# Kernel optimization log

Hardware: AMD Instinct MI355X
Metric: run time of the kernel (lower is better)

The kernel has to match this reference:

```python
import jax, jax.numpy as jnp
import numpy as np

B = 1024
NIF = 2048   # n_image_features
V = 10000    # vocab_size
E = 512      # embedding_dim
H = 1024     # hidden_size
L = 32       # max_sentence_length
ND = 3       # num distractors


def _lstm_cell(x, h, c, Wih, Whh, bih, bhh):
    # torch LSTMCell: gates ordered i, f, g, o
    g = x @ Wih.T + bih + h @ Whh.T + bhh
    i, f, gc, o = jnp.split(g, 4, axis=-1)
    c = jax.nn.sigmoid(f) * c + jax.nn.sigmoid(i) * jnp.tanh(gc)
    h = jax.nn.sigmoid(o) * jnp.tanh(c)
    return h, c


def setup_inputs() -> dict:
    key = jax.random.key(0)
    ks = jax.random.split(key, 20)
    s = 0.02
    inp = {
        "target": jax.random.normal(ks[0], (B, NIF), jnp.float32),
        "distractors": jax.random.normal(ks[1], (ND, B, NIF), jnp.float32),
        "start_token_idx": 1,
        "max_sentence_length": L,
        # Sender params
        "W_aff": s * jax.random.normal(ks[2], (H, NIF), jnp.float32),
        "b_aff": jnp.zeros((H,), jnp.float32),
        "emb_s": s * jax.random.normal(ks[3], (V, E), jnp.float32),
        "Wih_s": s * jax.random.normal(ks[4], (4 * H, E), jnp.float32),
        "Whh_s": s * jax.random.normal(ks[5], (4 * H, H), jnp.float32),
        "bih_s": jnp.zeros((4 * H,), jnp.float32),
        "bhh_s": jnp.zeros((4 * H,), jnp.float32),
        "Wp": s * jax.random.normal(ks[6], (V, H), jnp.float32),
        "bp": jnp.zeros((V,), jnp.float32),
        # Receiver params
        "emb_r": s * jax.random.normal(ks[7], (V, E), jnp.float32),
        "Wih_r": s * jax.random.normal(ks[8], (4 * H, E), jnp.float32),
        "Whh_r": s * jax.random.normal(ks[9], (4 * H, H), jnp.float32),
        "bih_r": jnp.zeros((4 * H,), jnp.float32),
        "bhh_r": jnp.zeros((4 * H,), jnp.float32),
        "W_out": s * jax.random.normal(ks[10], (NIF, H), jnp.float32),
        "b_out": jnp.zeros((NIF,), jnp.float32),
    }
    return inp


def reference(target, distractors, start_token_idx, max_sentence_length,
              W_aff, b_aff, emb_s, Wih_s, Whh_s, bih_s, bhh_s, Wp, bp,
              emb_r, Wih_r, Whh_r, bih_r, bhh_r, W_out, b_out):
    Bt = target.shape[0]

    # ---- Sender: greedy decode (eval-mode argmax, matching greedy=True) ----
    h0 = target @ W_aff.T + b_aff
    c0 = jnp.zeros_like(h0)
    w0 = emb_s[jnp.full((Bt,), start_token_idx, dtype=jnp.int32)]

    def send_step(carry, _):
        h, c, w = carry
        h, c = _lstm_cell(w, h, c, Wih_s, Whh_s, bih_s, bhh_s)
        logits = h @ Wp.T + bp                         # [B, V]
        idx = jnp.argmax(logits, axis=-1)              # greedy token
        logp = jnp.take_along_axis(jax.nn.log_softmax(logits, axis=-1),
                                   idx[:, None], axis=-1)[:, 0]
        w = emb_s[idx]
        return (h, c, w), (idx, logp)

    _, (message, logps) = jax.lax.scan(send_step, (h0, c0, w0), None,
                                       length=max_sentence_length)
    message = message.T            # [B, L]
    log_prob = logps[-1]           # log_prob of last sampled word, [B]

    # ---- Receiver: encode message ----
    hr = jnp.zeros((Bt, H), jnp.float32)
    cr = jnp.zeros((Bt, H), jnp.float32)

    def recv_step(carry, w_idx):
        h, c = carry
        h, c = _lstm_cell(emb_r[w_idx], h, c, Wih_r, Whh_r, bih_r, bhh_r)
        return (h, c), None

    (hr, cr), _ = jax.lax.scan(recv_step, (hr, cr), message.T)
    r = hr @ W_out.T + b_out       # [B, NIF]

    # ---- Hinge loss over distractors ----
    r_T = r.T                                       # [NIF, B]
    t_r = target @ r_T                              # [B, B]
    d_r = jnp.einsum('nbf,fc->nbc', distractors, r_T)  # [ND, B, B]
    loss = jnp.sum(jnp.maximum(0.0, 1.0 - t_r[None] + d_r), axis=0)  # [B, B]
    loss = -loss * log_prob        # broadcast [B] over last dim, as in torch
    return jnp.mean(loss)
```

## Files before the change

### kernel.cpp

```cpp
#include <hip/hip_runtime.h>
#include <hip/hip_bf16.h>
#include <cstdint>
#include <cstddef>

#define Bc   1024
#define NIFc 2048
#define Vc   10000
#define Ec   512
#define Hc   1024
#define Lc   32
#define NDc  3
#define G4c  4096
#define NTv  79
#define TMLD 80
#define XLD  3584
#define XOFF 512

typedef __attribute__((ext_vector_type(4))) float f32x4;
typedef __attribute__((ext_vector_type(8))) short s16x8;
typedef __attribute__((ext_vector_type(4))) short s16x4;

#define GBM 128
#define GBN 128
#define GBK 64

struct __align__(16) GemmSmem {
    __hip_bfloat16 As[GBM * GBK];
    __hip_bfloat16 Ws[GBN * GBK];
    float smax[GBM];
};

__device__ __forceinline__ void gld_lds16(void* lds, const void* g) {
    __builtin_amdgcn_global_load_lds(
        (const __attribute__((address_space(1))) unsigned int*)g,
        (__attribute__((address_space(3))) unsigned int*)lds,
        16, 0, 0);
}

template<int OBF>
__device__ __forceinline__ void gemm_body(
    GemmSmem& sm,
    const __hip_bfloat16* __restrict__ A, int lda,
    const __hip_bfloat16* __restrict__ W, int ldw,
// ... 66 lines not shown
                    acc[i][j] = __builtin_amdgcn_mfma_f32_16x16x32_bf16(
                        af[i], wf[j], acc[i][j], 0, 0, 0);
        }
    }

    float rowmax[4][4];
    #pragma unroll
    for (int i = 0; i < 4; ++i)
        #pragma unroll
        for (int rr = 0; rr < 4; ++rr)
            rowmax[i][rr] = -__builtin_inff();

    #pragma unroll
    for (int i = 0; i < 4; ++i) {
        int mbase = m0 + hm + i * 16 + quad * 4;
        #pragma unroll
        for (int j = 0; j < 4; ++j) {
            int n = n0 + hn + j * 16 + lm;
            if (n < N) {
                float bv = bias ? bias[n] : 0.0f;
                #pragma unroll
                for (int rr = 0; rr < 4; ++rr) {
                    float v = acc[i][j][rr] + bv;
                    if (mbase + rr < M) {
                        if (OBF)
                            ((__hip_bfloat16*)Cv)[(size_t)(mbase + rr) * N + n] =
                                __float2bfloat16(v);
                        else
                            ((float*)Cv)[(size_t)(mbase + rr) * N + n] = v;
                    }
                    rowmax[i][rr] = fmaxf(rowmax[i][rr], v);
                }
            }
        }
    }

    if (tile_max) {
        #pragma unroll
        for (int i = 0; i < 4; ++i)
            #pragma unroll
            for (int rr = 0; rr < 4; ++rr) {
                float v = rowmax[i][rr];
                v = fmaxf(v, __shfl_xor(v, 1));
                v = fmaxf(v, __shfl_xor(v, 2));
                v = fmaxf(v, __shfl_xor(v, 4));
                v = fmaxf(v, __shfl_xor(v, 8));
                rowmax[i][rr] = v;
            }
        __syncthreads();
        if (hn == 0 && lm == 0) {
            #pragma unroll
            for (int i = 0; i < 4; ++i)
                #pragma unroll
                for (int rr = 0; rr < 4; ++rr)
                    smax[hm + i * 16 + quad * 4 + rr] = rowmax[i][rr];
        }
        __syncthreads();
        if (hn == 64 && lm == 0) {
            #pragma unroll
            for (int i = 0; i < 4; ++i)
                #pragma unroll
                for (int rr = 0; rr < 4; ++rr) {
                    int r = hm + i * 16 + quad * 4 + rr;
                    smax[r] = fmaxf(smax[r], rowmax[i][rr]);
                }
        }
        __syncthreads();
        if (tid < GBM)
            tile_max[(size_t)(m0 + tid) * tmld + bx] = smax[tid];
    }
}

__global__ __launch_bounds__(256) void gemm_bf16_tn(
    const __hip_bfloat16* __restrict__ A, int lda,
    const __hip_bfloat16* __restrict__ W, int ldw,
    const float* __restrict__ bias, float* __restrict__ C,
    int M, int N, int K, float* __restrict__ tile_max, int tmld)
{
    __shared__ GemmSmem sm;
    gemm_body<0>(sm, A, lda, W, ldw, bias, C, M, N, K, blockIdx.x, blockIdx.y,
                 tile_max, tmld);
}

__global__ __launch_bounds__(256) void gemm_bf16_obf(
    const __hip_bfloat16* __restrict__ A, int lda,
    const __hip_bfloat16* __restrict__ W, int ldw,
    __hip_bfloat16* __restrict__ C, int M, int N, int K)
{
    __shared__ GemmSmem sm;
    gemm_body<1>(sm, A, lda, W, ldw, nullptr, C, M, N, K, blockIdx.x,
                 blockIdx.y, nullptr, 0);
}

__global__ __launch_bounds__(256) void gemm_bf16_sk2(
    const __hip_bfloat16* __restrict__ A, int lda,
    const __hip_bfloat16* __restrict__ W, int ldw,
    float* __restrict__ Cpart, int M, int N, int Ksub)
{
    __shared__ GemmSmem sm;
    int z = blockIdx.z;
    gemm_body<0>(sm, A + (size_t)z * Ksub, lda, W + (size_t)z * Ksub, ldw,
                 nullptr, Cpart + (size_t)z * M * N, M, N, Ksub, blockIdx.x,
                 blockIdx.y, nullptr, 0);
}

__global__ __launch_bounds__(256) void gemm_fused_step(
    int nb_g, int nb_l,
    const __hip_bfloat16* __restrict__ Ag, const __hip_bfloat16* __restrict__ Wg,
    float* __restrict__ Cg,
    const __hip_bfloat16* __restrict__ Al, const __hip_bfloat16* __restrict__ Wl,
    const float* __restrict__ bl, float* __restrict__ Cl,
    float* __restrict__ tmax,
    const __hip_bfloat16* __restrict__ Ar, const __hip_bfloat16* __restrict__ Wr,
    float* __restrict__ Cr)
{
    __shared__ GemmSmem sm;
    int bid = blockIdx.x;
    if (bid < nb_g) {
        gemm_body<0>(sm, Ag, XLD, Wg, XLD, nullptr, Cg,
                     Bc, G4c, 3072, bid & 31, bid >> 5, nullptr, 0);
    } else if (bid < nb_g + nb_l) {
        int rem = bid - nb_g;
        int by = rem / NTv, bx = rem - by * NTv;
        gemm_body<0>(sm, Al, XLD, Wl, Hc, bl, Cl, Bc, Vc, Hc, bx, by,
                     tmax, TMLD);
    } else {
        int rem = bid - nb_g - nb_l;
        gemm_body<0>(sm, Ar, 1536, Wr, 1536, nullptr, Cr,
                     Bc, G4c, Hc, rem & 31, rem >> 5, nullptr, 0);
    }
}

__global__ __launch_bounds__(256) void split3_a_kernel(
    const float* __restrict__ in, int ldin,
    __hip_bfloat16* __restrict__ out, int ldo, int coff, int M, int K)
{
    int i = blockIdx.x * 256 + threadIdx.x;
    if (i >= M * K) return;
    int m = i / K, k = i - m * K;
    float v = in[(size_t)m * ldin + k];
    __hip_bfloat16 hi = __float2bfloat16(v);
    float lo = v - __bfloat162float(hi);
    __hip_bfloat16* row = out + (size_t)m * ldo + coff;
    row[k] = hi;
    row[K + k] = __float2bfloat16(lo);
    row[2 * K + k] = hi;
}

__global__ __launch_bounds__(256) void split3_w_kernel(
    const float* __restrict__ in, int ldin,
    __hip_bfloat16* __restrict__ out, int ldo, int coff, int M, int K)
{
    int i = blockIdx.x * 256 + threadIdx.x;
    if (i >= M * K) return;
    int m = i / K, k = i - m * K;
    float v = in[(size_t)m * ldin + k];
    __hip_bfloat16 hi = __float2bfloat16(v);
    float lo = v - __bfloat162float(hi);
    __hip_bfloat16* row = out + (size_t)m * ldo + coff;
    row[k] = hi;
    row[K + k] = hi;
    row[2 * K + k] = __float2bfloat16(lo);
}

__global__ __launch_bounds__(256) void cast2d_kernel(
    const float* __restrict__ in, int ldin,
    __hip_bfloat16* __restrict__ out, int ldo, int coff, int M, int K)
{
    int i = blockIdx.x * 256 + threadIdx.x;
    if (i >= M * K) return;
    int m = i / K, k = i - m * K;
    out[(size_t)m * ldo + coff + k] = __float2bfloat16(in[(size_t)m * ldin + k]);
}

__global__ __launch_bounds__(256) void gather_cast_kernel(
    const float* __restrict__ emb, int E, const int* __restrict__ idx,
    int stride, __hip_bfloat16* __restrict__ out, int ldo, int coff, int Brows)
{
    int i = blockIdx.x * 256 + threadIdx.x;
    if (i >= Brows * E) return;
    int b = i / E, k = i - b * E;
    out[(size_t)b * ldo + coff + k] =
        __float2bfloat16(emb[(size_t)idx[(size_t)b * stride] * E + k]);
}

__global__ __launch_bounds__(256) void add_vec_kernel(
    const float* __restrict__ a, const float* __restrict__ b,
    float* __restrict__ o, int n)
{
    int i = blockIdx.x * 256 + threadIdx.x;
    if (i < n) o[i] = a[i] + b[i];
}

__device__ __forceinline__ short bf16bits(float x) {
    __hip_bfloat16 t = __float2bfloat16(x);
    return *reinterpret_cast<short*>(&t);
}

__device__ __forceinline__ float b16f(short s) {
    return __bfloat162float(*reinterpret_cast<__hip_bfloat16*>(&s));
}

__global__ __launch_bounds__(256) void lstm_fused_s(
    const float* __restrict__ gp0, const float* __restrict__ gp1,
    const float* __restrict__ bias, float* __restrict__ h,
    float* __restrict__ c, __hip_bfloat16* __restrict__ h3x,
    const __hip_bfloat16* __restrict__ xg, const int* __restrict__ tok,
    int tstride)
{
    int i = blockIdx.x * 256 + threadIdx.x;
    if (i >= Bc * Hc / 4) return;
    int b = i >> 8;
    int j = (i & 255) * 4;
    size_t g0 = (size_t)b * G4c + j;
// ... 59 lines not shown
    s16x4 hi4, lo4;
    #pragma unroll
    for (int k = 0; k < 4; ++k) {
        hi4[k] = bf16bits(v[k]);
        lo4[k] = bf16bits(v[k] - __bfloat162float(__float2bfloat16(v[k])));
    }
    __hip_bfloat16* row = h3x + (size_t)b * XLD + XOFF;
    *(s16x4*)(row + j) = hi4;
    *(s16x4*)(row + Hc + j) = lo4;
    *(s16x4*)(row + 2 * Hc + j) = hi4;
}

__global__ __launch_bounds__(256) void lstm_fused_r(
    const float* __restrict__ gp0, const float* __restrict__ gp1,
    const float* __restrict__ bias, float* __restrict__ h,
    float* __restrict__ c, __hip_bfloat16* __restrict__ xh_r,
    const __hip_bfloat16* __restrict__ xg, const int* __restrict__ tok,
    int has_g, const float* __restrict__ emb, const int* __restrict__ msg_next)
{
    int i = blockIdx.x * 256 + threadIdx.x;
    if (i >= Bc * Hc / 4) return;
    int b = i >> 8;
    int j = (i & 255) * 4;
    f32x4 gi = *(const f32x4*)(bias + j);
    f32x4 gf = *(const f32x4*)(bias + Hc + j);
    f32x4 gg = *(const f32x4*)(bias + 2 * Hc + j);
    f32x4 go = *(const f32x4*)(bias + 3 * Hc + j);
    if (has_g) {
        size_t g0 = (size_t)b * G4c + j;
        gi += *(const f32x4*)(gp0 + g0) + *(const f32x4*)(gp1 + g0);
        gf += *(const f32x4*)(gp0 + g0 + Hc) + *(const f32x4*)(gp1 + g0 + Hc);
        gg += *(const f32x4*)(gp0 + g0 + 2 * Hc) + *(const f32x4*)(gp1 + g0 + 2 * Hc);
        go += *(const f32x4*)(gp0 + g0 + 3 * Hc) + *(const f32x4*)(gp1 + g0 + 3 * Hc);
    }
    if (xg) {
        const __hip_bfloat16* xr = xg + (size_t)tok[b] * G4c;
        s16x4 xi = *(const s16x4*)(xr + j);
        s16x4 xf = *(const s16x4*)(xr + Hc + j);
        s16x4 xc = *(const s16x4*)(xr + 2 * Hc + j);
        s16x4 xo = *(const s16x4*)(xr + 3 * Hc + j);
        #pragma unroll
        for (int k = 0; k < 4; ++k) {
            gi[k] += b16f(xi[k]);
            gf[k] += b16f(xf[k]);
            gg[k] += b16f(xc[k]);
            go[k] += b16f(xo[k]);
        }
    }
    size_t hix = (size_t)b * Hc + j;
    f32x4 cv = *(const f32x4*)(c + hix);
    f32x4 cn, hv;
    s16x4 hb4;
    #pragma unroll
    for (int k = 0; k < 4; ++k) {
        float si = 1.0f / (1.0f + expf(-gi[k]));
        float sf = 1.0f / (1.0f + expf(-gf[k]));
        float so = 1.0f / (1.0f + expf(-go[k]));
        float cc = sf * cv[k] + si * tanhf(gg[k]);
        cn[k] = cc;
        float hh = so * tanhf(cc);
        hv[k] = hh;
        hb4[k] = bf16bits(hh);
    }
    *(f32x4*)(c + hix) = cn;
    *(f32x4*)(h + hix) = hv;
    *(s16x4*)(xh_r + (size_t)b * 1536 + Ec + j) = hb4;
    if (!xg && msg_next && j < Ec) {
        int t2 = msg_next[b];
        f32x4 e = *(const f32x4*)(emb + (size_t)t2 * Ec + j);
        s16x4 eb;
        #pragma unroll
        for (int k = 0; k < 4; ++k) eb[k] = bf16bits(e[k]);
        *(s16x4*)(xh_r + (size_t)b * 1536 + j) = eb;
    }
}

__global__ __launch_bounds__(256) void argmax_rescore_v3(
    const float* __restrict__ logits, const float* __restrict__ tmax,
    const float* __restrict__ h, const float* __restrict__ Wp,
    const float* __restrict__ bp, const float* __restrict__ emb,
    int* __restrict__ msg_t, float* __restrict__ logp,
    __hip_bfloat16* __restrict__ xdst, int want_logp)
{
    const int b = blockIdx.x;
    const int tid = threadIdx.x;
    const int lane = tid & 63;
    const int wave = tid >> 6;
    const float* row = logits + (size_t)b * Vc;

    __shared__ float stm[128];
    __shared__ float redm[256];
    __shared__ float reds[256];
    __shared__ int   qt[32];
    __shared__ int   nq, cnt;
    __shared__ int   cand[64];
    __shared__ float score[64];
// ... 84 lines not shown
            f32x4 v = row4[j];
            s += expf(v.x - m) + expf(v.y - m) + expf(v.z - m) + expf(v.w - m);
        }
        redm[tid] = s;
        __syncthreads();
        #pragma unroll
        for (int st = 128; st > 0; st >>= 1) {
            if (tid < st) redm[tid] += redm[tid + st];
            __syncthreads();
        }
        if (tid == 0) logp[b] = sbestv - (m + logf(redm[0]));
    }

    if (xdst && tid < 128) {
        int k = tid * 4;
        f32x4 e = *(const f32x4*)(emb + (size_t)bestj * Ec + k);
        s16x4 h4;
        #pragma unroll
        for (int kk = 0; kk < 4; ++kk) h4[kk] = bf16bits(e[kk]);
        *(s16x4*)(xdst + (size_t)b * XLD + k) = h4;
    }
}

__global__ __launch_bounds__(256) void argmax_lstm_step(
    const float* __restrict__ logits, const float* __restrict__ tmax,
    const float* __restrict__ h, const float* __restrict__ Wp,
    const float* __restrict__ bp, int* __restrict__ msg_t,
    float* __restrict__ logp, int want_logp,
    int do_s, const float* __restrict__ gp0,
    const float* __restrict__ bias_s, float* __restrict__ h_s,
    float* __restrict__ c_s, __hip_bfloat16* __restrict__ h3x,
    const __hip_bfloat16* __restrict__ Xg_s,
    int has_gr, const float* __restrict__ gr0,
    const float* __restrict__ bias_r, float* __restrict__ hr,
    float* __restrict__ cr, __hip_bfloat16* __restrict__ xh_r,
    const __hip_bfloat16* __restrict__ Xg_r)
{
    const int b = blockIdx.x;
    const int tid = threadIdx.x;
    const int lane = tid & 63;
    const int wave = tid >> 6;
    const float* row = logits + (size_t)b * Vc;

    __shared__ float stm[128];
    __shared__ float redm[256];
    __shared__ float reds[256];
    __shared__ int   qt[32];
    __shared__ int   nq, cnt;
    __shared__ int   cand[64];
    __shared__ float score[64];
    __shared__ float sbestv;
    __shared__ int   sbestj;

    float tv = (tid < NTv) ? tmax[(size_t)b * TMLD + tid] : -__builtin_inff();
    if (tid < 128) stm[tid] = tv;
    redm[tid] = tv;
    reds[tid] = (tid < NTv) ? tv : 0.0f;
    if (tid == 0) { nq = 0; cnt = 0; }
    __syncthreads();
    #pragma unroll
    for (int s = 128; s > 0; s >>= 1) {
        if (tid < s) {
            redm[tid] = fmaxf(redm[tid], redm[tid + s]);
            reds[tid] += reds[tid + s];
        }
        __syncthreads();
    }
    const float m = redm[0];
    const float spread = m - reds[0] * (1.0f / NTv);
    const float delta = 0.08f * spread + 1e-6f * (1.0f + fabsf(m));

    if (tid < NTv && stm[tid] >= m - delta) {
        int k = atomicAdd(&nq, 1);
        if (k < 32) qt[k] = tid;
    }
    __syncthreads();
    int nqt = nq < 32 ? nq : 32;

    for (int qi = 0; qi < nqt; qi += 2) {
        int ti = qi + (tid >> 7);
        if (ti < nqt) {
            int j = qt[ti] * 128 + (tid & 127);
            if (j < Vc) {
                float v = row[j];
                if (v >= m - delta) {
                    int k = atomicAdd(&cnt, 1);
                    if (k < 64) cand[k] = j;
                }
            }
        }
    }
    __syncthreads();
    int nc = cnt < 64 ? cnt : 64;

    const float* hrow = h + (size_t)b * Hc;
    for (int cix = wave; cix < nc; cix += 4) {
        int j = cand[cix];
        const float* wrow = Wp + (size_t)j * Hc;
        float part = 0.0f;
        #pragma unroll
        for (int kk = 0; kk < 4; ++kk) {
            int k = kk * 256 + lane * 4;
            f32x4 hv = *(const f32x4*)(hrow + k);
            f32x4 wv = *(const f32x4*)(wrow + k);
            part = fmaf(hv.x, wv.x, part);
            part = fmaf(hv.y, wv.y, part);
            part = fmaf(hv.z, wv.z, part);
            part = fmaf(hv.w, wv.w, part);
        }
        #pragma unroll
        for (int off = 1; off < 64; off <<= 1)
            part += __shfl_xor(part, off);
        if (lane == 0) score[cix] = part + bp[j];
    }
    __syncthreads();
    if (tid == 0) {
        float bv = -__builtin_inff();
        int bj = 0x7fffffff;
        for (int cix = 0; cix < nc; ++cix) {
            float v = score[cix];
            int j = cand[cix];
            if (v > bv || (v == bv && j < bj)) { bv = v; bj = j; }
        }
        sbestv = bv;
        sbestj = bj;
        msg_t[b] = bj;
    }
    __syncthreads();
    const int tok = sbestj;

    if (want_logp) {
        float s = 0.0f;
        const f32x4* row4 = (const f32x4*)row;
        for (int j = tid; j < Vc / 4; j += 256) {
            f32x4 v = row4[j];
            s += expf(v.x - m) + expf(v.y - m) + expf(v.z - m) + expf(v.w - m);
        }
        redm[tid] = s;
        __syncthreads();
        #pragma unroll
        for (int st = 128; st > 0; st >>= 1) {
            if (tid < st) redm[tid] += redm[tid + st];
            __syncthreads();
        }
        if (tid == 0) logp[b] = sbestv - (m + logf(redm[0]));
        __syncthreads();
    }

    const int j = tid * 4;

    if (do_s) {
        size_t g0 = (size_t)b * G4c + j;
        f32x4 gi = *(const f32x4*)(gp0 + g0) + *(const f32x4*)(bias_s + j);
        f32x4 gf = *(const f32x4*)(gp0 + g0 + Hc) + *(const f32x4*)(bias_s + Hc + j);
        f32x4 gg = *(const f32x4*)(gp0 + g0 + 2 * Hc) + *(const f32x4*)(bias_s + 2 * Hc + j);
        f32x4 go = *(const f32x4*)(gp0 + g0 + 3 * Hc) + *(const f32x4*)(bias_s + 3 * Hc + j);
        const __hip_bfloat16* xr = Xg_s + (size_t)tok * G4c;
        s16x4 xi = *(const s16x4*)(xr + j);
        s16x4 xf = *(const s16x4*)(xr + Hc + j);
        s16x4 xc = *(const s16x4*)(xr + 2 * Hc + j);
        s16x4 xo = *(const s16x4*)(xr + 3 * Hc + j);
        size_t hix = (size_t)b * Hc + j;
        f32x4 cv = *(const f32x4*)(c_s + hix);
        f32x4 cn, hv;
        s16x4 hi4, lo4;
        #pragma unroll
        for (int k = 0; k < 4; ++k) {
            float gik = gi[k] + b16f(xi[k]);
            float gfk = gf[k] + b16f(xf[k]);
            float ggk = gg[k] + b16f(xc[k]);
            float gok = go[k] + b16f(xo[k]);
            float si = 1.0f / (1.0f + expf(-gik));
            float sf = 1.0f / (1.0f + expf(-gfk));
            float so = 1.0f / (1.0f + expf(-gok));
            float cc = sf * cv[k] + si * tanhf(ggk);
            cn[k] = cc;
            float hh = so * tanhf(cc);
            hv[k] = hh;
            hi4[k] = bf16bits(hh);
            lo4[k] = bf16bits(hh - __bfloat162float(__float2bfloat16(hh)));
        }
        *(f32x4*)(c_s + hix) = cn;
        *(f32x4*)(h_s + hix) = hv;
        __hip_bfloat16* orow = h3x + (size_t)b * XLD + XOFF;
        *(s16x4*)(orow + j) = hi4;
        *(s16x4*)(orow + Hc + j) = lo4;
        *(s16x4*)(orow + 2 * Hc + j) = hi4;
    }

    {
        f32x4 gi = *(const f32x4*)(bias_r + j);
        f32x4 gf = *(const f32x4*)(bias_r + Hc + j);
        f32x4 gg = *(const f32x4*)(bias_r + 2 * Hc + j);
        f32x4 go = *(const f32x4*)(bias_r + 3 * Hc + j);
        if (has_gr) {
            size_t g0 = (size_t)b * G4c + j;
            gi += *(const f32x4*)(gr0 + g0);
            gf += *(const f32x4*)(gr0 + g0 + Hc);
            gg += *(const f32x4*)(gr0 + g0 + 2 * Hc);
            go += *(const f32x4*)(gr0 + g0 + 3 * Hc);
        }
        const __hip_bfloat16* xr = Xg_r + (size_t)tok * G4c;
        s16x4 xi = *(const s16x4*)(xr + j);
        s16x4 xf = *(const s16x4*)(xr + Hc + j);
        s16x4 xc = *(const s16x4*)(xr + 2 * Hc + j);
        s16x4 xo = *(const s16x4*)(xr + 3 * Hc + j);
        size_t hix = (size_t)b * Hc + j;
        f32x4 cv = *(const f32x4*)(cr + hix);
        f32x4 cn, hv;
        s16x4 hb4;
        #pragma unroll
        for (int k = 0; k < 4; ++k) {
            float gik = gi[k] + b16f(xi[k]);
            float gfk = gf[k] + b16f(xf[k]);
            float ggk = gg[k] + b16f(xc[k]);
            float gok = go[k] + b16f(xo[k]);
            float si = 1.0f / (1.0f + expf(-gik));
            float sf = 1.0f / (1.0f + expf(-gfk));
            float so = 1.0f / (1.0f + expf(-gok));
            float cc = sf * cv[k] + si * tanhf(ggk);
            cn[k] = cc;
            float hh = so * tanhf(cc);
            hv[k] = hh;
            hb4[k] = bf16bits(hh);
        }
        *(f32x4*)(cr + hix) = cn;
        *(f32x4*)(hr + hix) = hv;
        *(s16x4*)(xh_r + (size_t)b * 1536 + Ec + j) = hb4;
    }
}

__global__ __launch_bounds__(256) void hinge_kernel(
    const float* __restrict__ S, const float* __restrict__ logp,
    float* __restrict__ partials, int Bn)
{
    int tid = threadIdx.x;
    int n = Bn * Bn;
    float acc = 0.0f;
    for (int idx = blockIdx.x * 256 + tid; idx < n; idx += gridDim.x * 256) {
        int j = idx & (Bn - 1);
        float s0 = S[idx];
        float l = fmaxf(0.0f, 1.0f - s0 + S[n + idx])
                + fmaxf(0.0f, 1.0f - s0 + S[2 * n + idx])
                + fmaxf(0.0f, 1.0f - s0 + S[3 * n + idx]);
        acc += l * logp[j];
    }
    __shared__ float sv[256];
    sv[tid] = acc;
    __syncthreads();
    for (int s = 128; s > 0; s >>= 1) {
        if (tid < s) sv[tid] += sv[tid + s];
// ... 37 lines not shown
    const float* bhh_s = (const float*)d_in[10];
    const float* Wp    = (const float*)d_in[11];
    const float* bp    = (const float*)d_in[12];
    const float* emb_r = (const float*)d_in[13];
    const float* Wih_r = (const float*)d_in[14];
    const float* Whh_r = (const float*)d_in[15];
    const float* bih_r = (const float*)d_in[16];
    const float* bhh_r = (const float*)d_in[17];
    const float* W_out = (const float*)d_in[18];
    const float* b_out = (const float*)d_in[19];

    dim3 blk(256);

    char* b0 = (char*)d_ws;
    size_t off = 0;
    auto take = [&](size_t bytes) -> char* {
        char* p = b0 + off;
        off += (bytes + 511) & ~(size_t)511;
        return p;
    };
    const size_t MB = 1024 * 1024;
    __hip_bfloat16* W3x     = (__hip_bfloat16*)take((size_t)G4c * XLD * 2);
    __hip_bfloat16* Wp_b    = (__hip_bfloat16*)take((size_t)Vc * Hc * 2);
    __hip_bfloat16* WihWhh_r= (__hip_bfloat16*)take((size_t)G4c * 1536 * 2);
    __hip_bfloat16* W_out_b = (__hip_bfloat16*)take((size_t)NIFc * Hc * 2);
    __hip_bfloat16* h3x     = (__hip_bfloat16*)take((size_t)Bc * XLD * 2);
    __hip_bfloat16* xh_r    = (__hip_bfloat16*)take((size_t)Bc * 1536 * 2);
    float* gates_p = (float*)take((size_t)2 * Bc * G4c * 4);
    float* h_s    = (float*)take((size_t)Bc * Hc * 4);
    float* c_s    = (float*)take((size_t)Bc * Hc * 4);
    float* hr     = (float*)take((size_t)Bc * Hc * 4);
    float* cr     = (float*)take((size_t)Bc * Hc * 4);
    float* logp   = (float*)take(Bc * 4);
    int*   msg    = (int*)take((size_t)Lc * Bc * 4);
    float* parts  = (float*)take(1024 * 4);
    float* bias_s = (float*)take(G4c * 4);
    float* bias_r = (float*)take(G4c * 4);
    float* tilemax= (float*)take((size_t)Bc * TMLD * 4);
    char*  U      = take(48 * MB);

    __hip_bfloat16* Xg_s = (__hip_bfloat16*)take((size_t)Vc * G4c * 2);
    const int use_tab_s = (off <= ws_size);
    __hip_bfloat16* Xg_r = (__hip_bfloat16*)take((size_t)Vc * G4c * 2);
    const int use_tab_r = (off <= ws_size);
    const int use_merged = use_tab_s && use_tab_r;

    __hip_bfloat16* target3 = (__hip_bfloat16*)U;
    __hip_bfloat16* W_aff3  = (__hip_bfloat16*)(U + 13 * MB);
    __hip_bfloat16* emb_b   = (__hip_bfloat16*)(U + 26 * MB);
    float*          logits  = (float*)U;
    __hip_bfloat16* A4b     = (__hip_bfloat16*)U;
    float*          r_f     = (float*)(U + 17 * MB);
    __hip_bfloat16* r_b     = (__hip_bfloat16*)(U + 26 * MB);
    float*          S       = (float*)(U + 31 * MB);

    cast2d_kernel<<<(G4c * Ec + 255) / 256, blk, 0, stream>>>(
        Wih_s, Ec, W3x, XLD, 0, G4c, Ec);
    split3_w_kernel<<<(G4c * Hc + 255) / 256, blk, 0, stream>>>(
        Whh_s, Hc, W3x, XLD, XOFF, G4c, Hc);
    cast2d_kernel<<<(Vc * Hc + 255) / 256, blk, 0, stream>>>(
        Wp, Hc, Wp_b, Hc, 0, Vc, Hc);
    split3_a_kernel<<<(Bc * NIFc + 255) / 256, blk, 0, stream>>>(
        target, NIFc, target3, 6144, 0, Bc, NIFc);
    split3_w_kernel<<<(Hc * NIFc + 255) / 256, blk, 0, stream>>>(
        W_aff, NIFc, W_aff3, 6144, 0, Hc, NIFc);
    cast2d_kernel<<<(G4c * Ec + 255) / 256, blk, 0, stream>>>(
        Wih_r, Ec, WihWhh_r, 1536, 0, G4c, Ec);
    cast2d_kernel<<<(G4c * Hc + 255) / 256, blk, 0, stream>>>(
        Whh_r, Hc, WihWhh_r, 1536, Ec, G4c, Hc);
    cast2d_kernel<<<(NIFc * Hc + 255) / 256, blk, 0, stream>>>(
        W_out, Hc, W_out_b, Hc, 0, NIFc, Hc);
    add_vec_kernel<<<(G4c + 255) / 256, blk, 0, stream>>>(bih_s, bhh_s,
                                                          bias_s, G4c);
    add_vec_kernel<<<(G4c + 255) / 256, blk, 0, stream>>>(bih_r, bhh_r,
                                                          bias_r, G4c);

    if (use_tab_s) {
        cast2d_kernel<<<(Vc * Ec + 255) / 256, blk, 0, stream>>>(
            emb_s, Ec, emb_b, Ec, 0, Vc, Ec);
        gemm_bf16_obf<<<dim3(G4c / GBN, (Vc + GBM - 1) / GBM), blk, 0, stream>>>(
            emb_b, Ec, W3x, XLD, Xg_s, Vc, G4c, Ec);
    }
    if (use_tab_r) {
        cast2d_kernel<<<(Vc * Ec + 255) / 256, blk, 0, stream>>>(
            emb_r, Ec, emb_b, Ec, 0, Vc, Ec);
        gemm_bf16_obf<<<dim3(G4c / GBN, (Vc + GBM - 1) / GBM), blk, 0, stream>>>(
            emb_b, Ec, WihWhh_r, 1536, Xg_r, Vc, G4c, Ec);
    }

    gemm_bf16_sk2<<<dim3(Hc / GBN, Bc / GBM, 2), blk, 0, stream>>>(
        target3, 6144, W_aff3, 6144, gates_p, Bc, Hc, 3072);
    combine_h0_kernel<<<(Bc * Hc / 4 + 255) / 256, blk, 0, stream>>>(
        gates_p, gates_p + (size_t)Bc * Hc, b_aff, h_s, h3x);
    hipMemsetAsync(c_s, 0, (size_t)Bc * Hc * 4, stream);

    if (use_merged) {
        hipMemsetAsync(cr, 0, (size_t)Bc * Hc * 4, stream);

        gemm_bf16_sk2<<<dim3(G4c / GBN, Bc / GBM, 2), blk, 0, stream>>>(
            h3x + XOFF, XLD, W3x + XOFF, XLD, gates_p, Bc, G4c, 1536);
        lstm_fused_s<<<(Bc * Hc / 4 + 255) / 256, blk, 0, stream>>>(
            gates_p, gates_p + (size_t)Bc * G4c, bias_s, h_s, c_s, h3x,
            Xg_s, start_t, 0);

        float* gates_s = gates_p;
        float* gates_r = gates_p + (size_t)Bc * G4c;

        for (int t = 0; t < Lc; ++t) {
            const int nb_g = (t < Lc - 1) ? 256 : 0;
            const int nb_r = (t >= 1) ? 256 : 0;
            gemm_fused_step<<<nb_g + 632 + nb_r, blk, 0, stream>>>(
                nb_g, 632,
                h3x + XOFF, W3x + XOFF, gates_s,
                h3x + XOFF, Wp_b, bp, logits, tilemax,
                xh_r + Ec, WihWhh_r + Ec, gates_r);
            argmax_lstm_step<<<Bc, blk, 0, stream>>>(
                logits, tilemax, h_s, Wp, bp, msg + t * Bc, logp,
                (t == Lc - 1) ? 1 : 0,
                (t < Lc - 1) ? 1 : 0, gates_s, bias_s, h_s, c_s, h3x, Xg_s,
                (t >= 1) ? 1 : 0, gates_r, bias_r, hr, cr, xh_r, Xg_r);
        }
    } else {
        if (!use_tab_s)
            gather_cast_kernel<<<(Bc * Ec + 255) / 256, blk, 0, stream>>>(
                emb_s, Ec, start_t, 0, h3x, XLD, 0, Bc);

        for (int t = 0; t < Lc; ++t) {
            if (use_tab_s) {
                gemm_bf16_sk2<<<dim3(G4c / GBN, Bc / GBM, 2), blk, 0, stream>>>(
                    h3x + XOFF, XLD, W3x + XOFF, XLD, gates_p, Bc, G4c, 1536);
                lstm_fused_s<<<(Bc * Hc / 4 + 255) / 256, blk, 0, stream>>>(
                    gates_p, gates_p + (size_t)Bc * G4c, bias_s, h_s, c_s, h3x,
                    Xg_s, (t == 0) ? start_t : (msg + (t - 1) * Bc),
                    (t == 0) ? 0 : 1);
            } else {
                gemm_bf16_sk2<<<dim3(G4c / GBN, Bc / GBM, 2), blk, 0, stream>>>(
                    h3x, XLD, W3x, XLD, gates_p, Bc, G4c, 1792);
                lstm_fused_s<<<(Bc * Hc / 4 + 255) / 256, blk, 0, stream>>>(
                    gates_p, gates_p + (size_t)Bc * G4c, bias_s, h_s, c_s, h3x,
                    nullptr, nullptr, 0);
            }
            gemm_bf16_tn<<<dim3((Vc + GBN - 1) / GBN, Bc / GBM), blk, 0, stream>>>(
                h3x + XOFF, XLD, Wp_b, Hc, bp, logits, Bc, Vc, Hc, tilemax, TMLD);
            argmax_rescore_v3<<<Bc, blk, 0, stream>>>(
                logits, tilemax, h_s, Wp, bp, emb_s, msg + t * Bc, logp,
                (!use_tab_s && t < Lc - 1) ? h3x : nullptr,
                (t == Lc - 1) ? 1 : 0);
        }

        hipMemsetAsync(hr, 0, (size_t)Bc * Hc * 4, stream);
        hipMemsetAsync(cr, 0, (size_t)Bc * Hc * 4, stream);
        hipMemsetAsync(xh_r, 0, (size_t)Bc * 1536 * 2, stream);
        if (!use_tab_r)
            gather_cast_kernel<<<(Bc * Ec + 255) / 256, blk, 0, stream>>>(
                emb_r, Ec, msg, 1, xh_r, 1536, 0, Bc);
        for (int t = 0; t < Lc; ++t) {
            if (use_tab_r) {
                if (t > 0)
                    gemm_bf16_sk2<<<dim3(G4c / GBN, Bc / GBM, 2), blk, 0, stream>>>(
                        xh_r + Ec, 1536, WihWhh_r + Ec, 1536, gates_p, Bc, G4c, 512);
                lstm_fused_r<<<(Bc * Hc / 4 + 255) / 256, blk, 0, stream>>>(
                    gates_p, gates_p + (size_t)Bc * G4c, bias_r, hr, cr, xh_r,
                    Xg_r, msg + t * Bc, (t > 0) ? 1 : 0, nullptr, nullptr);
            } else {
                gemm_bf16_sk2<<<dim3(G4c / GBN, Bc / GBM, 2), blk, 0, stream>>>(
                    xh_r, 1536, WihWhh_r, 1536, gates_p, Bc, G4c, 768);
                lstm_fused_r<<<(Bc * Hc / 4 + 255) / 256, blk, 0, stream>>>(
                    gates_p, gates_p + (size_t)Bc * G4c, bias_r, hr, cr, xh_r,
                    nullptr, nullptr, 1, emb_r,
                    (t < Lc - 1) ? (msg + (t + 1) * Bc) : nullptr);
            }
        }
    }

    gemm_bf16_tn<<<dim3(NIFc / GBN, Bc / GBM), blk, 0, stream>>>(
        xh_r + Ec, 1536, W_out_b, Hc, b_out, r_f, Bc, NIFc, Hc, nullptr, 0);

    cast2d_kernel<<<(Bc * NIFc + 255) / 256, blk, 0, stream>>>(
        target, NIFc, A4b, NIFc, 0, Bc, NIFc);
    cast2d_kernel<<<(NDc * Bc * NIFc + 255) / 256, blk, 0, stream>>>(
        distr, NIFc, A4b + (size_t)Bc * NIFc, NIFc, 0, NDc * Bc, NIFc);
    cast2d_kernel<<<(Bc * NIFc + 255) / 256, blk, 0, stream>>>(
        r_f, NIFc, r_b, NIFc, 0, Bc, NIFc);
    gemm_bf16_tn<<<dim3(Bc / GBN, 4 * Bc / GBM), blk, 0, stream>>>(
        A4b, NIFc, r_b, NIFc, nullptr, S, 4 * Bc, Bc, NIFc, nullptr, 0);

    hinge_kernel<<<1024, blk, 0, stream>>>(S, logp, parts, Bc);
    final_reduce_kernel<<<1, blk, 0, stream>>>(
        parts, 1024, (float*)d_out, -1.0f / ((float)Bc * (float)Bc));
}
```

Before: 4.510 ms.

## Fuse receiver LSTM cell into gate GEMM epilogue and store sender logits as bf16

The receiver's gate weights are permuted so each 64-column GEMM tile holds all four gates for 16 hidden units. The LSTM cell update can then run in the GEMM epilogue, with ping-pong h buffers and a final standalone recv kernel. This removes the fp32 receiver gate round-trip and the receiver cell work in the argmax kernel. Sender logits for non-final steps are written as bf16, halving logit traffic, and the tile max is computed on rounded values. The trade-offs are bf16 rounding in the argmax candidate screen and a heavier epilogue with gathered Xg reads.

```diff
diff --git a/kernel.cpp b/kernel.cpp
--- a/kernel.cpp
+++ b/kernel.cpp
@@ -15,10 +15,15 @@
 #define TMLD 80
 #define XLD  3584
 #define XOFF 512
+#define RLD  1536
 
 typedef __attribute__((ext_vector_type(4))) float f32x4;
 typedef __attribute__((ext_vector_type(8))) short s16x8;
 typedef __attribute__((ext_vector_type(4))) short s16x4;
+
+__device__ __host__ __forceinline__ int rperm_orig(int p) {
+    return ((p >> 4) & 3) * Hc + (p >> 6) * 16 + (p & 15);
+}
 
 #define GBM 128
 #define GBN 128
@@ -131,14 +136,17 @@
                 #pragma unroll
                 for (int rr = 0; rr < 4; ++rr) {
                     float v = acc[i][j][rr] + bv;
-                    if (mbase + rr < M) {
-                        if (OBF)
-                            ((__hip_bfloat16*)Cv)[(size_t)(mbase + rr) * N + n] =
-                                __float2bfloat16(v);
-                        else
+                    float vs = v;
+                    if (OBF) {
+                        __hip_bfloat16 vb = __float2bfloat16(v);
+                        vs = __bfloat162float(vb);
+                        if (mbase + rr < M)
+                            ((__hip_bfloat16*)Cv)[(size_t)(mbase + rr) * N + n] = vb;
+                    } else {
+                        if (mbase + rr < M)
                             ((float*)Cv)[(size_t)(mbase + rr) * N + n] = v;
                     }
-                    rowmax[i][rr] = fmaxf(rowmax[i][rr], v);
+                    rowmax[i][rr] = fmaxf(rowmax[i][rr], vs);
                 }
             }
         }
@@ -180,6 +188,120 @@
     }
 }
 
+__device__ __forceinline__ void recv_gemm_cell_body(
+    GemmSmem& sm,
+    const __hip_bfloat16* __restrict__ A,
+    const __hip_bfloat16* __restrict__ W,
+    const float* __restrict__ biasp,
+    const __hip_bfloat16* __restrict__ Xg,
+    const int* __restrict__ tok,
+    float* __restrict__ cr,
+    __hip_bfloat16* __restrict__ xh_out,
+    int bx, int by)
+{
+    __hip_bfloat16* As = sm.As;
+    __hip_bfloat16* Ws = sm.Ws;
+
+    const int tid  = threadIdx.x;
+    const int lane = tid & 63;
+    const int wave = tid >> 6;
+    const int m0 = by * GBM;
+    const int n0 = bx * GBN;
+
+    const __hip_bfloat16* ag[4];
+    const __hip_bfloat16* wg[4];
+    #pragma unroll
+    for (int r = 0; r < 4; ++r) {
+        int p = r * 256 + tid;
+        int m = p >> 3;
+        int q = (p & 7) ^ (m & 7);
+        ag[r] = A + (size_t)(m0 + m) * RLD + q * 8;
+        wg[r] = W + (size_t)(n0 + m) * RLD + q * 8;
+    }
+
+    f32x4 acc[4][4];
+    #pragma unroll
+    for (int i = 0; i < 4; ++i)
+        #pragma unroll
+        for (int j = 0; j < 4; ++j)
+            acc[i][j] = (f32x4)(0.0f);
+
+    const int hm = (wave & 1) << 6;
+    const int hn = (wave >> 1) << 6;
+    const int lm = lane & 15;
+    const int quad = lane >> 4;
+
+    for (int kt = 0; kt < Hc / GBK; ++kt) {
+        __syncthreads();
+        #pragma unroll
+        for (int r = 0; r < 4; ++r) {
+            int ldsbase = (r * 256 + wave * 64) * 8;
+            gld_lds16(As + ldsbase, ag[r]);
+            gld_lds16(Ws + ldsbase, wg[r]);
+            ag[r] += GBK;
+            wg[r] += GBK;
+        }
+        __syncthreads();
+        #pragma unroll
+        for (int c = 0; c < 2; ++c) {
+            s16x8 af[4], wf[4];
+            int q = c * 4 + quad;
+            #pragma unroll
+            for (int i = 0; i < 4; ++i) {
+                int m = hm + i * 16 + lm;
+                af[i] = *(const s16x8*)(As + ((m << 3) + (q ^ (m & 7))) * 8);
+                int n = hn + i * 16 + lm;
+                wf[i] = *(const s16x8*)(Ws + ((n << 3) + (q ^ (n & 7))) * 8);
+            }
+            #pragma unroll
+            for (int i = 0; i < 4; ++i)
+                #pragma unroll
+                for (int j = 0; j < 4; ++j)
+                    acc[i][j] = __builtin_amdgcn_mfma_f32_16x16x32_bf16(
+                        af[i], wf[j], acc[i][j], 0, 0, 0);
+        }
+    }
+
+    const int u = ((n0 + hn) >> 6) * 16 + lm;
+    int pc[4];
+    float bv[4];
+    #pragma unroll
+    for (int g = 0; g < 4; ++g) {
+        pc[g] = n0 + hn + g * 16 + lm;
+        bv[g] = biasp[pc[g]];
+    }
+    #pragma unroll
+    for (int i = 0; i < 4; ++i) {
+        #pragma unroll
+        for (int rr = 0; rr < 4; ++rr) {
+            int b = m0 + hm + i * 16 + quad * 4 + rr;
+            const __hip_bfloat16* xr = Xg + (size_t)tok[b] * G4c;
+            float gi = acc[i][0][rr] + bv[0] + __bfloat162float(xr[pc[0]]);
+            float gf = acc[i][1][rr] + bv[1] + __bfloat162float(xr[pc[1]]);
+            float gg = acc[i][2][rr] + bv[2] + __bfloat162float(xr[pc[2]]);
+            float go = acc[i][3][rr] + bv[3] + __bfloat162float(xr[pc[3]]);
+            float si = 1.0f / (1.0f + expf(-gi));
+            float sf = 1.0f / (1.0f + expf(-gf));
+            float so = 1.0f / (1.0f + expf(-go));
+            size_t cix = (size_t)b * Hc + u;
+            float cc = sf * cr[cix] + si * tanhf(gg);
+            cr[cix] = cc;
+            xh_out[(size_t)b * RLD + Ec + u] = __float2bfloat16(so * tanhf(cc));
+        }
+    }
+}
+
+__global__ __launch_bounds__(256) void gemm_recv_final(
+    const __hip_bfloat16* __restrict__ A, const __hip_bfloat16* __restrict__ W,
+    const float* __restrict__ biasp, const __hip_bfloat16* __restrict__ Xg,
+    const int* __restrict__ tok, float* __restrict__ cr,
+    __hip_bfloat16* __restrict__ xh_out)
+{
+    __shared__ GemmSmem sm;
+    recv_gemm_cell_body(sm, A, W, biasp, Xg, tok, cr, xh_out,
+                        blockIdx.x & 31, blockIdx.x >> 5);
+}
+
 __global__ __launch_bounds__(256) void gemm_bf16_tn(
     const __hip_bfloat16* __restrict__ A, int lda,
     const __hip_bfloat16* __restrict__ W, int ldw,
@@ -213,30 +335,33 @@
                  blockIdx.y, nullptr, 0);
 }
 
+template<int LOGBF>
 __global__ __launch_bounds__(256) void gemm_fused_step(
-    int nb_g, int nb_l,
+    int nb_g,
     const __hip_bfloat16* __restrict__ Ag, const __hip_bfloat16* __restrict__ Wg,
     float* __restrict__ Cg,
     const __hip_bfloat16* __restrict__ Al, const __hip_bfloat16* __restrict__ Wl,
-    const float* __restrict__ bl, float* __restrict__ Cl,
+    const float* __restrict__ bl, void* __restrict__ Cl,
     float* __restrict__ tmax,
     const __hip_bfloat16* __restrict__ Ar, const __hip_bfloat16* __restrict__ Wr,
-    float* __restrict__ Cr)
+    const float* __restrict__ biasrp, const __hip_bfloat16* __restrict__ Xgr,
+    const int* __restrict__ tokr, float* __restrict__ cr,
+    __hip_bfloat16* __restrict__ xh_out)
 {
     __shared__ GemmSmem sm;
     int bid = blockIdx.x;
     if (bid < nb_g) {
         gemm_body<0>(sm, Ag, XLD, Wg, XLD, nullptr, Cg,
                      Bc, G4c, 3072, bid & 31, bid >> 5, nullptr, 0);
-    } else if (bid < nb_g + nb_l) {
+    } else if (bid < nb_g + 632) {
         int rem = bid - nb_g;
         int by = rem / NTv, bx = rem - by * NTv;
-        gemm_body<0>(sm, Al, XLD, Wl, Hc, bl, Cl, Bc, Vc, Hc, bx, by,
-                     tmax, TMLD);
+        gemm_body<LOGBF>(sm, Al, XLD, Wl, Hc, bl, Cl, Bc, Vc, Hc, bx, by,
+                         tmax, TMLD);
     } else {
-        int rem = bid - nb_g - nb_l;
-        gemm_body<0>(sm, Ar, 1536, Wr, 1536, nullptr, Cr,
-                     Bc, G4c, Hc, rem & 31, rem >> 5, nullptr, 0);
+        int rem = bid - nb_g - 632;
+        recv_gemm_cell_body(sm, Ar, Wr, biasrp, Xgr, tokr, cr, xh_out,
+                            rem & 31, rem >> 5);
     }
 }
 
@@ -282,6 +407,17 @@
     out[(size_t)m * ldo + coff + k] = __float2bfloat16(in[(size_t)m * ldin + k]);
 }
 
+__global__ __launch_bounds__(256) void cast2d_perm_kernel(
+    const float* __restrict__ in, int ldin,
+    __hip_bfloat16* __restrict__ out, int ldo, int coff, int M, int K)
+{
+    int i = blockIdx.x * 256 + threadIdx.x;
+    if (i >= M * K) return;
+    int p = i / K, k = i - p * K;
+    out[(size_t)p * ldo + coff + k] =
+        __float2bfloat16(in[(size_t)rperm_orig(p) * ldin + k]);
+}
+
 __global__ __launch_bounds__(256) void gather_cast_kernel(
     const float* __restrict__ emb, int E, const int* __restrict__ idx,
     int stride, __hip_bfloat16* __restrict__ out, int ldo, int coff, int Brows)
@@ -299,6 +435,14 @@
 {
     int i = blockIdx.x * 256 + threadIdx.x;
     if (i < n) o[i] = a[i] + b[i];
+}
+
+__global__ __launch_bounds__(256) void add_vec_perm_kernel(
+    const float* __restrict__ a, const float* __restrict__ b,
+    float* __restrict__ o, int n)
+{
+    int i = blockIdx.x * 256 + threadIdx.x;
+    if (i < n) { int s = rperm_orig(i); o[i] = a[s] + b[s]; }
 }
 
 __device__ __forceinline__ short bf16bits(float x) {
@@ -404,23 +548,24 @@
     if (i >= Bc * Hc / 4) return;
     int b = i >> 8;
     int j = (i & 255) * 4;
-    f32x4 gi = *(const f32x4*)(bias + j);
-    f32x4 gf = *(const f32x4*)(bias + Hc + j);
-    f32x4 gg = *(const f32x4*)(bias + 2 * Hc + j);
-    f32x4 go = *(const f32x4*)(bias + 3 * Hc + j);
+    int pb = (j >> 4) * 64 + (j & 15);
+    f32x4 gi = *(const f32x4*)(bias + pb);
+    f32x4 gf = *(const f32x4*)(bias + pb + 16);
+    f32x4 gg = *(const f32x4*)(bias + pb + 32);
+    f32x4 go = *(const f32x4*)(bias + pb + 48);
     if (has_g) {
-        size_t g0 = (size_t)b * G4c + j;
+        size_t g0 = (size_t)b * G4c + pb;
         gi += *(const f32x4*)(gp0 + g0) + *(const f32x4*)(gp1 + g0);
-        gf += *(const f32x4*)(gp0 + g0 + Hc) + *(const f32x4*)(gp1 + g0 + Hc);
-        gg += *(const f32x4*)(gp0 + g0 + 2 * Hc) + *(const f32x4*)(gp1 + g0 + 2 * Hc);
-        go += *(const f32x4*)(gp0 + g0 + 3 * Hc) + *(const f32x4*)(gp1 + g0 + 3 * Hc);
+        gf += *(const f32x4*)(gp0 + g0 + 16) + *(const f32x4*)(gp1 + g0 + 16);
+        gg += *(const f32x4*)(gp0 + g0 + 32) + *(const f32x4*)(gp1 + g0 + 32);
+        go += *(const f32x4*)(gp0 + g0 + 48) + *(const f32x4*)(gp1 + g0 + 48);
     }
     if (xg) {
         const __hip_bfloat16* xr = xg + (size_t)tok[b] * G4c;
-        s16x4 xi = *(const s16x4*)(xr + j);
-        s16x4 xf = *(const s16x4*)(xr + Hc + j);
-        s16x4 xc = *(const s16x4*)(xr + 2 * Hc + j);
-        s16x4 xo = *(const s16x4*)(xr + 3 * Hc + j);
+        s16x4 xi = *(const s16x4*)(xr + pb);
+        s16x4 xf = *(const s16x4*)(xr + pb + 16);
+        s16x4 xc = *(const s16x4*)(xr + pb + 32);
+        s16x4 xo = *(const s16x4*)(xr + pb + 48);
         #pragma unroll
         for (int k = 0; k < 4; ++k) {
             gi[k] += b16f(xi[k]);
@@ -446,14 +591,14 @@
     }
     *(f32x4*)(c + hix) = cn;
     *(f32x4*)(h + hix) = hv;
-    *(s16x4*)(xh_r + (size_t)b * 1536 + Ec + j) = hb4;
+    *(s16x4*)(xh_r + (size_t)b * RLD + Ec + j) = hb4;
     if (!xg && msg_next && j < Ec) {
         int t2 = msg_next[b];
         f32x4 e = *(const f32x4*)(emb + (size_t)t2 * Ec + j);
         s16x4 eb;
         #pragma unroll
         for (int k = 0; k < 4; ++k) eb[k] = bf16bits(e[k]);
-        *(s16x4*)(xh_r + (size_t)b * 1536 + j) = eb;
+        *(s16x4*)(xh_r + (size_t)b * RLD + j) = eb;
     }
 }
 
@@ -584,25 +729,23 @@
     }
 }
 
+template<int LGBF>
 __global__ __launch_bounds__(256) void argmax_lstm_step(
-    const float* __restrict__ logits, const float* __restrict__ tmax,
+    const void* __restrict__ logits_v, const float* __restrict__ tmax,
     const float* __restrict__ h, const float* __restrict__ Wp,
     const float* __restrict__ bp, int* __restrict__ msg_t,
     float* __restrict__ logp, int want_logp,
     int do_s, const float* __restrict__ gp0,
     const float* __restrict__ bias_s, float* __restrict__ h_s,
     float* __restrict__ c_s, __hip_bfloat16* __restrict__ h3x,
-    const __hip_bfloat16* __restrict__ Xg_s,
-    int has_gr, const float* __restrict__ gr0,
-    const float* __restrict__ bias_r, float* __restrict__ hr,
-    float* __restrict__ cr, __hip_bfloat16* __restrict__ xh_r,
-    const __hip_bfloat16* __restrict__ Xg_r)
+    const __hip_bfloat16* __restrict__ Xg_s)
 {
     const int b = blockIdx.x;
     const int tid = threadIdx.x;
     const int lane = tid & 63;
     const int wave = tid >> 6;
-    const float* row = logits + (size_t)b * Vc;
+    const __hip_bfloat16* rowb = (const __hip_bfloat16*)logits_v + (size_t)b * Vc;
+    const float* rowf = (const float*)logits_v + (size_t)b * Vc;
 
     __shared__ float stm[128];
     __shared__ float redm[256];
@@ -644,7 +787,7 @@
         if (ti < nqt) {
             int j = qt[ti] * 128 + (tid & 127);
             if (j < Vc) {
-                float v = row[j];
+                float v = LGBF ? __bfloat162float(rowb[j]) : rowf[j];
                 if (v >= m - delta) {
                     int k = atomicAdd(&cnt, 1);
                     if (k < 64) cand[k] = j;
@@ -691,9 +834,9 @@
     __syncthreads();
     const int tok = sbestj;
 
-    if (want_logp) {
+    if (!LGBF && want_logp) {
         float s = 0.0f;
-        const f32x4* row4 = (const f32x4*)row;
+        const f32x4* row4 = (const f32x4*)rowf;
         for (int j = tid; j < Vc / 4; j += 256) {
             f32x4 v = row4[j];
             s += expf(v.x - m) + expf(v.y - m) + expf(v.z - m) + expf(v.w - m);
@@ -709,9 +852,8 @@
         __syncthreads();
     }
 
-    const int j = tid * 4;
-
     if (do_s) {
+        const int j = tid * 4;
         size_t g0 = (size_t)b * G4c + j;
         f32x4 gi = *(const f32x4*)(gp0 + g0) + *(const f32x4*)(bias_s + j);
         f32x4 gf = *(const f32x4*)(gp0 + g0 + Hc) + *(const f32x4*)(bias_s + Hc + j);
@@ -748,47 +890,6 @@
         *(s16x4*)(orow + j) = hi4;
         *(s16x4*)(orow + Hc + j) = lo4;
         *(s16x4*)(orow + 2 * Hc + j) = hi4;
-    }
-
-    {
-        f32x4 gi = *(const f32x4*)(bias_r + j);
-        f32x4 gf = *(const f32x4*)(bias_r + Hc + j);
-        f32x4 gg = *(const f32x4*)(bias_r + 2 * Hc + j);
-        f32x4 go = *(const f32x4*)(bias_r + 3 * Hc + j);
-        if (has_gr) {
-            size_t g0 = (size_t)b * G4c + j;
-            gi += *(const f32x4*)(gr0 + g0);
-            gf += *(const f32x4*)(gr0 + g0 + Hc);
-            gg += *(const f32x4*)(gr0 + g0 + 2 * Hc);
-            go += *(const f32x4*)(gr0 + g0 + 3 * Hc);
-        }
-        const __hip_bfloat16* xr = Xg_r + (size_t)tok * G4c;
-        s16x4 xi = *(const s16x4*)(xr + j);
-        s16x4 xf = *(const s16x4*)(xr + Hc + j);
-        s16x4 xc = *(const s16x4*)(xr + 2 * Hc + j);
-        s16x4 xo = *(const s16x4*)(xr + 3 * Hc + j);
-        size_t hix = (size_t)b * Hc + j;
-        f32x4 cv = *(const f32x4*)(cr + hix);
-        f32x4 cn, hv;
-        s16x4 hb4;
-        #pragma unroll
-        for (int k = 0; k < 4; ++k) {
-            float gik = gi[k] + b16f(xi[k]);
-            float gfk = gf[k] + b16f(xf[k]);
-            float ggk = gg[k] + b16f(xc[k]);
-            float gok = go[k] + b16f(xo[k]);
-            float si = 1.0f / (1.0f + expf(-gik));
-            float sf = 1.0f / (1.0f + expf(-gfk));
-            float so = 1.0f / (1.0f + expf(-gok));
-            float cc = sf * cv[k] + si * tanhf(ggk);
-            cn[k] = cc;
-            float hh = so * tanhf(cc);
-            hv[k] = hh;
-            hb4[k] = bf16bits(hh);
-        }
-        *(f32x4*)(cr + hix) = cn;
-        *(f32x4*)(hr + hix) = hv;
-        *(s16x4*)(xh_r + (size_t)b * 1536 + Ec + j) = hb4;
     }
 }
 
@@ -872,10 +973,11 @@
     const size_t MB = 1024 * 1024;
     __hip_bfloat16* W3x     = (__hip_bfloat16*)take((size_t)G4c * XLD * 2);
     __hip_bfloat16* Wp_b    = (__hip_bfloat16*)take((size_t)Vc * Hc * 2);
-    __hip_bfloat16* WihWhh_r= (__hip_bfloat16*)take((size_t)G4c * 1536 * 2);
+    __hip_bfloat16* WihWhh_r= (__hip_bfloat16*)take((size_t)G4c * RLD * 2);
     __hip_bfloat16* W_out_b = (__hip_bfloat16*)take((size_t)NIFc * Hc * 2);
     __hip_bfloat16* h3x     = (__hip_bfloat16*)take((size_t)Bc * XLD * 2);
-    __hip_bfloat16* xh_r    = (__hip_bfloat16*)take((size_t)Bc * 1536 * 2);
+    __hip_bfloat16* xh_rA   = (__hip_bfloat16*)take((size_t)Bc * RLD * 2);
+    __hip_bfloat16* xh_rB   = (__hip_bfloat16*)take((size_t)Bc * RLD * 2);
     float* gates_p = (float*)take((size_t)2 * Bc * G4c * 4);
     float* h_s    = (float*)take((size_t)Bc * Hc * 4);
     float* c_s    = (float*)take((size_t)Bc * Hc * 4);
@@ -914,16 +1016,16 @@
         target, NIFc, target3, 6144, 0, Bc, NIFc);
     split3_w_kernel<<<(Hc * NIFc + 255) / 256, blk, 0, stream>>>(
         W_aff, NIFc, W_aff3, 6144, 0, Hc, NIFc);
-    cast2d_kernel<<<(G4c * Ec + 255) / 256, blk, 0, stream>>>(
-        Wih_r, Ec, WihWhh_r, 1536, 0, G4c, Ec);
-    cast2d_kernel<<<(G4c * Hc + 255) / 256, blk, 0, stream>>>(
-        Whh_r, Hc, WihWhh_r, 1536, Ec, G4c, Hc);
+    cast2d_perm_kernel<<<(G4c * Ec + 255) / 256, blk, 0, stream>>>(
+        Wih_r, Ec, WihWhh_r, RLD, 0, G4c, Ec);
+    cast2d_perm_kernel<<<(G4c * Hc + 255) / 256, blk, 0, stream>>>(
+        Whh_r, Hc, WihWhh_r, RLD, Ec, G4c, Hc);
     cast2d_kernel<<<(NIFc * Hc + 255) / 256, blk, 0, stream>>>(
         W_out, Hc, W_out_b, Hc, 0, NIFc, Hc);
     add_vec_kernel<<<(G4c + 255) / 256, blk, 0, stream>>>(bih_s, bhh_s,
                                                           bias_s, G4c);
-    add_vec_kernel<<<(G4c + 255) / 256, blk, 0, stream>>>(bih_r, bhh_r,
-                                                          bias_r, G4c);
+    add_vec_perm_kernel<<<(G4c + 255) / 256, blk, 0, stream>>>(bih_r, bhh_r,
+                                                               bias_r, G4c);
 
     if (use_tab_s) {
         cast2d_kernel<<<(Vc * Ec + 255) / 256, blk, 0, stream>>>(
@@ -935,7 +1037,7 @@
         cast2d_kernel<<<(Vc * Ec + 255) / 256, blk, 0, stream>>>(
             emb_r, Ec, emb_b, Ec, 0, Vc, Ec);
         gemm_bf16_obf<<<dim3(G4c / GBN, (Vc + GBM - 1) / GBM), blk, 0, stream>>>(
-            emb_b, Ec, WihWhh_r, 1536, Xg_r, Vc, G4c, Ec);
+            emb_b, Ec, WihWhh_r, RLD, Xg_r, Vc, G4c, Ec);
     }
 
     gemm_bf16_sk2<<<dim3(Hc / GBN, Bc / GBM, 2), blk, 0, stream>>>(
@@ -946,6 +1048,7 @@
 
     if (use_merged) {
         hipMemsetAsync(cr, 0, (size_t)Bc * Hc * 4, stream);
+        hipMemsetAsync(xh_rA, 0, (size_t)Bc * RLD * 2, stream);
 
         gemm_bf16_sk2<<<dim3(G4c / GBN, Bc / GBM, 2), blk, 0, stream>>>(
             h3x + XOFF, XLD, W3x + XOFF, XLD, gates_p, Bc, G4c, 1536);
@@ -953,23 +1056,38 @@
             gates_p, gates_p + (size_t)Bc * G4c, bias_s, h_s, c_s, h3x,
             Xg_s, start_t, 0);
 
-        float* gates_s = gates_p;
-        float* gates_r = gates_p + (size_t)Bc * G4c;
-
         for (int t = 0; t < Lc; ++t) {
-            const int nb_g = (t < Lc - 1) ? 256 : 0;
-            const int nb_r = (t >= 1) ? 256 : 0;
-            gemm_fused_step<<<nb_g + 632 + nb_r, blk, 0, stream>>>(
-                nb_g, 632,
-                h3x + XOFF, W3x + XOFF, gates_s,
-                h3x + XOFF, Wp_b, bp, logits, tilemax,
-                xh_r + Ec, WihWhh_r + Ec, gates_r);
-            argmax_lstm_step<<<Bc, blk, 0, stream>>>(
-                logits, tilemax, h_s, Wp, bp, msg + t * Bc, logp,
-                (t == Lc - 1) ? 1 : 0,
-                (t < Lc - 1) ? 1 : 0, gates_s, bias_s, h_s, c_s, h3x, Xg_s,
-                (t >= 1) ? 1 : 0, gates_r, bias_r, hr, cr, xh_r, Xg_r);
-        }
+            const int do_g = (t < Lc - 1);
+            const int do_r = (t >= 1);
+            const int k = t - 1;
+            const __hip_bfloat16* rin = (k & 1) ? xh_rB : xh_rA;
+            __hip_bfloat16* rout = (k & 1) ? xh_rA : xh_rB;
+            const int nb = do_g * 256 + 632 + do_r * 256;
+            if (t < Lc - 1) {
+                gemm_fused_step<1><<<nb, blk, 0, stream>>>(
+                    do_g ? 256 : 0,
+                    h3x + XOFF, W3x + XOFF, gates_p,
+                    h3x + XOFF, Wp_b, bp, (void*)logits, tilemax,
+                    do_r ? rin + Ec : nullptr, WihWhh_r + Ec, bias_r, Xg_r,
+                    do_r ? msg + (t - 1) * Bc : nullptr, cr, rout);
+                argmax_lstm_step<1><<<Bc, blk, 0, stream>>>(
+                    (const void*)logits, tilemax, h_s, Wp, bp, msg + t * Bc,
+                    logp, 0, 1, gates_p, bias_s, h_s, c_s, h3x, Xg_s);
+            } else {
+                gemm_fused_step<0><<<nb, blk, 0, stream>>>(
+                    0,
+                    h3x + XOFF, W3x + XOFF, gates_p,
+                    h3x + XOFF, Wp_b, bp, (void*)logits, tilemax,
+                    rin + Ec, WihWhh_r + Ec, bias_r, Xg_r,
+                    msg + (t - 1) * Bc, cr, rout);
+                argmax_lstm_step<0><<<Bc, blk, 0, stream>>>(
+                    (const void*)logits, tilemax, h_s, Wp, bp, msg + t * Bc,
+                    logp, 1, 0, gates_p, bias_s, h_s, c_s, h3x, Xg_s);
+            }
+        }
+        gemm_recv_final<<<256, blk, 0, stream>>>(
+            xh_rB + Ec, WihWhh_r + Ec, bias_r, Xg_r, msg + (Lc - 1) * Bc,
+            cr, xh_rA);
     } else {
         if (!use_tab_s)
             gather_cast_kernel<<<(Bc * Ec + 255) / 256, blk, 0, stream>>>(
@@ -1000,23 +1118,23 @@
 
         hipMemsetAsync(hr, 0, (size_t)Bc * Hc * 4, stream);
         hipMemsetAsync(cr, 0, (size_t)Bc * Hc * 4, stream);
-        hipMemsetAsync(xh_r, 0, (size_t)Bc * 1536 * 2, stream);
+        hipMemsetAsync(xh_rA, 0, (size_t)Bc * RLD * 2, stream);
         if (!use_tab_r)
             gather_cast_kernel<<<(Bc * Ec + 255) / 256, blk, 0, stream>>>(
-                emb_r, Ec, msg, 1, xh_r, 1536, 0, Bc);
+                emb_r, Ec, msg, 1, xh_rA, RLD, 0, Bc);
         for (int t = 0; t < Lc; ++t) {
             if (use_tab_r) {
                 if (t > 0)
                     gemm_bf16_sk2<<<dim3(G4c / GBN, Bc / GBM, 2), blk, 0, stream>>>(
-                        xh_r + Ec, 1536, WihWhh_r + Ec, 1536, gates_p, Bc, G4c, 512);
+                        xh_rA + Ec, RLD, WihWhh_r + Ec, RLD, gates_p, Bc, G4c, 512);
                 lstm_fused_r<<<(Bc * Hc / 4 + 255) / 256, blk, 0, stream>>>(
-                    gates_p, gates_p + (size_t)Bc * G4c, bias_r, hr, cr, xh_r,
+                    gates_p, gates_p + (size_t)Bc * G4c, bias_r, hr, cr, xh_rA,
                     Xg_r, msg + t * Bc, (t > 0) ? 1 : 0, nullptr, nullptr);
             } else {
                 gemm_bf16_sk2<<<dim3(G4c / GBN, Bc / GBM, 2), blk, 0, stream>>>(
-                    xh_r, 1536, WihWhh_r, 1536, gates_p, Bc, G4c, 768);
+                    xh_rA, RLD, WihWhh_r, RLD, gates_p, Bc, G4c, 768);
                 lstm_fused_r<<<(Bc * Hc / 4 + 255) / 256, blk, 0, stream>>>(
-                    gates_p, gates_p + (size_t)Bc * G4c, bias_r, hr, cr, xh_r,
+                    gates_p, gates_p + (size_t)Bc * G4c, bias_r, hr, cr, xh_rA,
                     nullptr, nullptr, 1, emb_r,
                     (t < Lc - 1) ? (msg + (t + 1) * Bc) : nullptr);
             }
@@ -1024,7 +1142,7 @@
     }
 
     gemm_bf16_tn<<<dim3(NIFc / GBN, Bc / GBM), blk, 0, stream>>>(
-        xh_r + Ec, 1536, W_out_b, Hc, b_out, r_f, Bc, NIFc, Hc, nullptr, 0);
+        xh_rA + Ec, RLD, W_out_b, Hc, b_out, r_f, Bc, NIFc, Hc, nullptr, 0);
 
     cast2d_kernel<<<(Bc * NIFc + 255) / 256, blk, 0, stream>>>(
         target, NIFc, A4b, NIFc, 0, Bc, NIFc);
```

New measurement: 4.504 ms. No clear change (-0.1%).
